# Kernel tuning notes

Measured on AMD Instinct MI355X. Metric: run time of the kernel, lower is better.

## Reference

```python
import jax, jax.numpy as jnp
import numpy as np

BN_EPS = 1e-5


def setup_inputs() -> dict:
    key = jax.random.key(0)
    ks = jax.random.split(key, 6)
    B, N, M, C1, C2 = 8, 8192, 2048, 128, 256
    in_ch = C1 + C2  # 384
    return {
        "xyz1": jax.random.uniform(ks[0], (B, N, 3), dtype=jnp.float32),
        "xyz2": jax.random.uniform(ks[1], (B, M, 3), dtype=jnp.float32),
        "features1": jax.random.normal(ks[2], (B, C1, N), dtype=jnp.float32),
        "features2": jax.random.normal(ks[3], (B, C2, M), dtype=jnp.float32),
        # Conv1d(kernel_size=1, bias=False) weights, squeezed to [out, in]
        "conv_w0": jax.random.normal(ks[4], (256, in_ch), dtype=jnp.float32) * 0.05,
        "gamma0": jnp.ones((256,), dtype=jnp.float32),
        "beta0": jnp.zeros((256,), dtype=jnp.float32),
        "conv_w1": jax.random.normal(ks[5], (256, 256), dtype=jnp.float32) * 0.05,
        "gamma1": jnp.ones((256,), dtype=jnp.float32),
        "beta1": jnp.zeros((256,), dtype=jnp.float32),
    }


def _conv_bn_relu(x, w, gamma, beta):
    # 1x1 Conv1d (no bias) == per-point channel matmul: [B,Cin,N] -> [B,Cout,N]
    x = jnp.einsum("oc,bcn->bon", w, x)
    # BatchNorm1d in training mode: batch stats over (B, N), biased variance
    mu = jnp.mean(x, axis=(0, 2), keepdims=True)
    var = jnp.var(x, axis=(0, 2), keepdims=True)
    x = (x - mu) * jax.lax.rsqrt(var + BN_EPS)
    x = x * gamma[None, :, None] + beta[None, :, None]
    return jax.nn.relu(x)


def reference(xyz1, xyz2, features1, features2,
              conv_w0, gamma0, beta0, conv_w1, gamma1, beta1):
    # squared pairwise distances [B, N, M] (broadcast diff reduced over coord dim)
    diff = xyz1[:, :, None, :] - xyz2[:, None, :, :]  # [B,N,M,3]
    dists = jnp.sum(diff * diff, axis=-1)             # [B,N,M]
    idx = jnp.argmin(dists, axis=-1)                  # [B,N] nearest downsampled point

    # per-batch gather: features2[b, :, idx[b]] -> [B, C2, N]
    interp = jax.vmap(lambda f, i: f[:, i])(features2, idx)

    x = jnp.concatenate([features1, interp], axis=1)  # [B, C1+C2, N]
    x = _conv_bn_relu(x, conv_w0, gamma0, beta0)
    x = _conv_bn_relu(x, conv_w1, gamma1, beta1)
    return x
```

## Files before the change

### kernel.cpp

```cpp
#include <hip/hip_runtime.h>
#include <stdint.h>

typedef unsigned short u16;
typedef unsigned int u32;
typedef __attribute__((ext_vector_type(8))) short short8;
typedef __attribute__((ext_vector_type(4))) float floatx4;

__device__ __forceinline__ u16 f2b(float f) {
  union { float f; u32 u; } c; c.f = f;
  u32 u = c.u;
  u += 0x7fffu + ((u >> 16) & 1u);
  return (u16)(u >> 16);
}
__device__ __forceinline__ float b2f(u16 h) {
  union { u32 u; float f; } c; c.u = ((u32)h) << 16;
  return c.f;
}

__device__ __forceinline__ void glds16(const void* g, void* l) {
  __builtin_amdgcn_global_load_lds((__attribute__((address_space(1))) void*)g,
                                   (__attribute__((address_space(3))) void*)l, 16, 0, 0);
}

__global__ void prep_all_k(const float* __restrict__ xyz1, const float* __restrict__ xyz2,
                           float2* __restrict__ cand,
                           const float* __restrict__ f1, u16* __restrict__ f1t,
                           const float* __restrict__ f2, u16* __restrict__ f2t,
                           const float* __restrict__ w0, u16* __restrict__ w0b,
                           const float* __restrict__ w1, u16* __restrict__ w1b,
                           float* __restrict__ sums) {
  __shared__ __align__(16) char smem[9216];
  int blk = blockIdx.x, t = threadIdx.x;
  if (blk < 512) {
    float4* s2 = (float4*)smem;
    int nq = blk & 7, mq = (blk >> 3) & 7, b = blk >> 6;
    const float* x2 = xyz2 + ((size_t)b * 2048 + mq * 256) * 3;
    s2[t] = make_float4(x2[t * 3], x2[t * 3 + 1], x2[t * 3 + 2], 0.f);
    __syncthreads();
    int n0 = nq * 1024 + t;
    float px[4], py[4], pz[4];
#pragma unroll
    for (int q = 0; q < 4; q++) {
      const float* p1 = xyz1 + ((size_t)b * 8192 + n0 + q * 256) * 3;
      px[q] = p1[0]; py[q] = p1[1]; pz[q] = p1[2];
    }
    float best[4] = {3.0e38f, 3.0e38f, 3.0e38f, 3.0e38f};
    int bi[4] = {0, 0, 0, 0};
#pragma unroll 4
    for (int m = 0; m < 256; m++) {
      float4 qq = s2[m];
#pragma unroll
      for (int q = 0; q < 4; q++) {
        float dx = px[q] - qq.x, dy = py[q] - qq.y, dz = pz[q] - qq.z;
        float d = fmaf(dz, dz, fmaf(dy, dy, dx * dx));
        bool c = d < best[q];
        best[q] = c ? d : best[q];
        bi[q] = c ? m : bi[q];
      }
    }
#pragma unroll
    for (int q = 0; q < 4; q++) {
      int n = n0 + q * 256;
      cand[(size_t)mq * 65536 + (size_t)b * 8192 + n] =
          make_float2(best[q], __int_as_float(mq * 256 + bi[q]));
    }
  } else if (blk < 3584) {
    const float* in; u16* out; int C, N, bx, by, bz;
    if (blk < 2560) { int rel = blk - 512;  in = f1; out = f1t; C = 128; N = 8192; bx = rel & 127; by = (rel >> 7) & 1; bz = rel >> 8; }
    else            { int rel = blk - 2560; in = f2; out = f2t; C = 256; N = 2048; bx = rel & 31;  by = (rel >> 5) & 3; bz = rel >> 7; }
    u16 (*tile)[72] = (u16(*)[72])smem;
    int c0 = by * 64, n0 = bx * 64;
    const float* src = in + ((size_t)bz * C + c0) * N + n0;
#pragma unroll
    for (int i = 0; i < 4; i++) {
      int id = t + i * 256;
      int c = id >> 4, nq = (id & 15) * 4;
      float4 v = *(const float4*)(src + (size_t)c * N + nq);
      tile[nq + 0][c] = f2b(v.x);
      tile[nq + 1][c] = f2b(v.y);
      tile[nq + 2][c] = f2b(v.z);
      tile[nq + 3][c] = f2b(v.w);
    }
    __syncthreads();
    int n = t >> 2, ch = (t & 3) * 16;
    u16* dst = out + ((size_t)bz * N + n0 + n) * C + c0 + ch;
    *(uint4*)dst = *(const uint4*)&tile[n][ch];
    *(uint4*)(dst + 8) = *(const uint4*)&tile[n][ch + 8];
  } else {
    int rel = blk - 3584;
    int i = rel * 256 + t;
    if (rel < 384) w0b[i] = f2b(w0[i]);
    else { int j = i - 98304; w1b[j] = f2b(w1[j]); }
    if (rel < 4) sums[i] = 0.f;
  }
}

__global__ __launch_bounds__(512, 2) void gemm1_k(const u16* __restrict__ w0b, const u16* __restrict__ f1t,
                                                  const u16* __restrict__ f2t, const float2* __restrict__ cand,
                                                  float* __restrict__ sum0, float* __restrict__ sq0,
                                                  u16* __restrict__ y0) {
  __shared__ u16 Aw[128 * 384];
  __shared__ u16 Bs[2][128 * 64];
  int t = threadIdx.x;
  int bid = blockIdx.x;
  int ohalf = (bid >> 3) & 1;
  int pairidx = (bid & 7) | ((bid >> 4) << 3);
  int o0 = ohalf * 128;
  int lane = t & 63, wave = t >> 6;
  int wrow = (wave >> 2) * 64;
  int wp = (wave & 3) * 32;
  int lr = lane & 15, lq = lane >> 4;
  int srow = lane >> 3;
  int sch = ((lane & 7) ^ srow) * 8;

#pragma unroll
  for (int it = 0; it < 12; it++) {
    u32 off = (u32)it * 8192 + (u32)t * 16;
    int row = off / 768;
    int c16 = (off - row * 768) >> 4;
    glds16(w0b + (size_t)(o0 + row) * 384 + ((c16 ^ (row & 7)) << 3),
           (char*)Aw + (size_t)it * 8192 + (size_t)wave * 1024);
  }

  float sa[4][4], qa[4][4];
#pragma unroll
  for (int i = 0; i < 4; i++)
#pragma unroll
    for (int r = 0; r < 4; r++) { sa[i][r] = 0.f; qa[i][r] = 0.f; }

  for (int s = 0; s < 4; s++) {
    int pt = pairidx * 4 + s;
    int pt0 = pt * 128;
    int b = pt0 >> 13;
    int gidx[2];
#pragma unroll
    for (int i = 0; i < 2; i++) {
      int p = pt0 + (wave * 2 + i) * 8 + srow;
      float bd = 3.0e38f; int bi = 0;
#pragma unroll
      for (int qc = 0; qc < 8; qc++) {
        float2 c = cand[(size_t)qc * 65536 + p];
        if (c.x < bd) { bd = c.x; bi = __float_as_int(c.y); }
      }
      gidx[i] = bi;
    }
    floatx4 zero = {0.f, 0.f, 0.f, 0.f};
    floatx4 acc[4][2];
#pragma unroll
    for (int i = 0; i < 4; i++)
#pragma unroll
      for (int j = 0; j < 2; j++) acc[i][j] = zero;

    auto stageB = [&](int k0, int bufi) {
      if (k0 < 128) {
#pragma unroll
        for (int i = 0; i < 2; i++)
          glds16(f1t + (size_t)(pt0 + (wave * 2 + i) * 8 + srow) * 128 + k0 + sch,
                 &Bs[bufi][(wave * 2 + i) * 512]);
      } else {
#pragma unroll
        for (int i = 0; i < 2; i++)
          glds16(f2t + ((size_t)(b << 11) + gidx[i]) * 256 + (k0 - 128) + sch,
                 &Bs[bufi][(wave * 2 + i) * 512]);
      }
    };
    auto compute = [&](int k0, int bufi) {
#pragma unroll
      for (int ks = 0; ks < 2; ks++) {
        short8 af[4], bf[2];
#pragma unroll
        for (int i = 0; i < 4; i++) {
          int row = wrow + i * 16 + lr;
          af[i] = *(const short8*)&Aw[row * 384 + ((((k0 >> 3) + (ks << 2) + lq) ^ (lr & 7)) << 3)];
        }
#pragma unroll
        for (int j = 0; j < 2; j++) {
          int row = wp + j * 16 + lr;
          bf[j] = *(const short8*)&Bs[bufi][row * 64 + ((((ks << 2) | lq) ^ (lr & 7)) << 3)];
        }
#pragma unroll
        for (int i = 0; i < 4; i++)
#pragma unroll
          for (int j = 0; j < 2; j++)
            acc[i][j] = __builtin_amdgcn_mfma_f32_16x16x32_bf16(af[i], bf[j], acc[i][j], 0, 0, 0);
      }
    };

    stageB(0, 0);
    __syncthreads();
#pragma unroll
    for (int k0i = 0; k0i < 6; k0i++) {
      if (k0i < 5) stageB((k0i + 1) * 64, (k0i + 1) & 1);
      compute(k0i * 64, k0i & 1);
      __syncthreads();
    }

#pragma unroll
    for (int i = 0; i < 4; i++) {
#pragma unroll
      for (int j = 0; j < 2; j++) {
        int o = o0 + wrow + i * 16 + lq * 4;
        int p = pt0 + wp + j * 16 + lr;
        uint2 pk;
        pk.x = (u32)f2b(acc[i][j][0]) | ((u32)f2b(acc[i][j][1]) << 16);
        pk.y = (u32)f2b(acc[i][j][2]) | ((u32)f2b(acc[i][j][3]) << 16);
        *(uint2*)&y0[(size_t)p * 256 + o] = pk;
      }
#pragma unroll
      for (int r = 0; r < 4; r++) {
        float v0 = acc[i][0][r], v1 = acc[i][1][r];
        sa[i][r] += v0 + v1;
        qa[i][r] += v0 * v0 + v1 * v1;
      }
    }
  }

#pragma unroll
  for (int i = 0; i < 4; i++)
#pragma unroll
    for (int r = 0; r < 4; r++)
#pragma unroll
      for (int m = 8; m >= 1; m >>= 1) {
        sa[i][r] += __shfl_xor(sa[i][r], m);
        qa[i][r] += __shfl_xor(qa[i][r], m);
      }
  __syncthreads();
  float* red = (float*)&Bs[0][0];
  if (t < 256) red[t] = 0.f;
  __syncthreads();
  if (lr == 0) {
#pragma unroll
    for (int i = 0; i < 4; i++)
#pragma unroll
      for (int r = 0; r < 4; r++) {
        int o = wrow + i * 16 + lq * 4 + r;
        atomicAdd(&red[o], sa[i][r]);
        atomicAdd(&red[128 + o], qa[i][r]);
      }
  }
  __syncthreads();
  if (t < 128) {
    atomicAdd(&sum0[o0 + t], red[t]);
    atomicAdd(&sq0[o0 + t], red[128 + t]);
  }
}

__global__ __launch_bounds__(512, 2) void gemm2_k(const u16* __restrict__ w1b, const u16* __restrict__ y0,
                                                  const float* __restrict__ sum0, const float* __restrict__ sq0,
                                                  const float* __restrict__ gamma0, const float* __restrict__ beta0,
                                                  float* __restrict__ sum1, float* __restrict__ sq1,
                                                  u16* __restrict__ y1) {
  __shared__ u16 Aw[128 * 256];
  __shared__ u16 Bs[2][256 * 64];
  __shared__ float ssc[256], ssh[256];
  int t = threadIdx.x;
  int bid = blockIdx.x;
  int ohalf = (bid >> 3) & 1;
  int pairidx = (bid & 7) | ((bid >> 4) << 3);
  int o0 = ohalf * 128;
  int lane = t & 63, wave = t >> 6;
  int wrow = (wave >> 2) * 64;
  int wp = (wave & 3) * 64;
  int lr = lane & 15, lq = lane >> 4;
  if (t < 256) {
    float mean = sum0[t] * (1.f / 65536.f);
    float var = fmaxf(sq0[t] * (1.f / 65536.f) - mean * mean, 0.f);
    float r = rsqrtf(var + 1e-5f);
    float sc = gamma0[t] * r;
    ssc[t] = sc;
    ssh[t] = beta0[t] - mean * sc;
  }
#pragma unroll
  for (int it = 0; it < 8; it++) {
    u32 off = (u32)it * 8192 + (u32)t * 16;
    int row = off >> 9;
    int c16 = (off & 511) >> 4;
    glds16(w1b + (size_t)(o0 + row) * 256 + ((c16 ^ (row & 7)) << 3),
           (char*)Aw + (size_t)it * 8192 + (size_t)wave * 1024);
  }

  int brow[4], bpc[4], bch[4];
#pragma unroll
  for (int i = 0; i < 4; i++) {
    int id = t + i * 512;
    brow[i] = id >> 3; bpc[i] = id & 7;
    bch[i] = (bpc[i] ^ (brow[i] & 7)) * 8;
  }
  float sa[4][4], qa[4][4];
#pragma unroll
  for (int i = 0; i < 4; i++)
#pragma unroll
    for (int r = 0; r < 4; r++) { sa[i][r] = 0.f; qa[i][r] = 0.f; }

  __syncthreads();

  for (int s = 0; s < 2; s++) {
    int pt0 = (pairidx * 2 + s) * 256;
    uint4 rg[4];
    auto loadB = [&](int k0) {
#pragma unroll
      for (int i = 0; i < 4; i++)
        rg[i] = *(const uint4*)(y0 + (size_t)(pt0 + brow[i]) * 256 + k0 + bch[i]);
    };
    auto xformB = [&](int k0, int bufi) {
#pragma unroll
      for (int i = 0; i < 4; i++) {
        u32 rw[4] = {rg[i].x, rg[i].y, rg[i].z, rg[i].w};
        u32 ow[4];
#pragma unroll
        for (int w = 0; w < 4; w++) {
          int k = k0 + bch[i] + w * 2;
          float v0 = b2f((u16)(rw[w] & 0xffffu));
          float v1 = b2f((u16)(rw[w] >> 16));
          v0 = fmaxf(v0 * ssc[k] + ssh[k], 0.f);
          v1 = fmaxf(v1 * ssc[k + 1] + ssh[k + 1], 0.f);
          ow[w] = (u32)f2b(v0) | ((u32)f2b(v1) << 16);
        }
        uint4 ov; ov.x = ow[0]; ov.y = ow[1]; ov.z = ow[2]; ov.w = ow[3];
        *(uint4*)&Bs[bufi][brow[i] * 64 + bpc[i] * 8] = ov;
      }
    };
    floatx4 zero = {0.f, 0.f, 0.f, 0.f};
    floatx4 acc[4][4];
#pragma unroll
    for (int i = 0; i < 4; i++)
#pragma unroll
      for (int j = 0; j < 4; j++) acc[i][j] = zero;
    auto compute = [&](int k0, int bufi) {
#pragma unroll
      for (int ks = 0; ks < 2; ks++) {
        short8 af[4], bf[4];
#pragma unroll
        for (int i = 0; i < 4; i++) {
          int row = wrow + i * 16 + lr;
          af[i] = *(const short8*)&Aw[row * 256 + ((((k0 >> 3) + (ks << 2) + lq) ^ (lr & 7)) << 3)];
        }
#pragma unroll
        for (int j = 0; j < 4; j++) {
          int row = wp + j * 16 + lr;
          bf[j] = *(const short8*)&Bs[bufi][row * 64 + ((((ks << 2) | lq) ^ (lr & 7)) << 3)];
        }
#pragma unroll
        for (int i = 0; i < 4; i++)
#pragma unroll
          for (int j = 0; j < 4; j++)
            acc[i][j] = __builtin_amdgcn_mfma_f32_16x16x32_bf16(af[i], bf[j], acc[i][j], 0, 0, 0);
      }
    };

    loadB(0);
    xformB(0, 0);
    __syncthreads();
#pragma unroll
    for (int k0i = 0; k0i < 4; k0i++) {
      if (k0i < 3) loadB((k0i + 1) * 64);
      compute(k0i * 64, k0i & 1);
      __syncthreads();
      if (k0i < 3) {
        xformB((k0i + 1) * 64, (k0i + 1) & 1);
        __syncthreads();
      }
    }
#pragma unroll
    for (int i = 0; i < 4; i++) {
#pragma unroll
      for (int j = 0; j < 4; j++) {
        int o = o0 + wrow + i * 16 + lq * 4;
        int p = pt0 + wp + j * 16 + lr;
        uint2 pk;
        pk.x = (u32)f2b(acc[i][j][0]) | ((u32)f2b(acc[i][j][1]) << 16);
        pk.y = (u32)f2b(acc[i][j][2]) | ((u32)f2b(acc[i][j][3]) << 16);
        *(uint2*)&y1[(size_t)p * 256 + o] = pk;
      }
#pragma unroll
      for (int r = 0; r < 4; r++) {
        float v0 = acc[i][0][r], v1 = acc[i][1][r], v2 = acc[i][2][r], v3 = acc[i][3][r];
        sa[i][r] += v0 + v1 + v2 + v3;
        qa[i][r] += v0 * v0 + v1 * v1 + v2 * v2 + v3 * v3;
      }
    }
  }

#pragma unroll
  for (int i = 0; i < 4; i++)
#pragma unroll
    for (int r = 0; r < 4; r++)
#pragma unroll
      for (int m = 8; m >= 1; m >>= 1) {
        sa[i][r] += __shfl_xor(sa[i][r], m);
        qa[i][r] += __shfl_xor(qa[i][r], m);
      }
  __syncthreads();
  float* red = (float*)&Bs[0][0];
  if (t < 256) red[t] = 0.f;
  __syncthreads();
  if (lr == 0) {
#pragma unroll
    for (int i = 0; i < 4; i++)
#pragma unroll
      for (int r = 0; r < 4; r++) {
        int o = wrow + i * 16 + lq * 4 + r;
        atomicAdd(&red[o], sa[i][r]);
        atomicAdd(&red[128 + o], qa[i][r]);
      }
  }
  __syncthreads();
  if (t < 128) {
    atomicAdd(&sum1[o0 + t], red[t]);
    atomicAdd(&sq1[o0 + t], red[128 + t]);
  }
}

__global__ void finalize_k(const u16* __restrict__ y1, const float* __restrict__ sum1,
                           const float* __restrict__ sq1, const float* __restrict__ gamma1,
                           const float* __restrict__ beta1, float* __restrict__ out) {
  __shared__ float tile[64][65];
  __shared__ float fs[64], fh[64];
  int b = blockIdx.z, o0 = blockIdx.y * 64, n0 = blockIdx.x * 64;
  int t = threadIdx.x;
  if (t < 64) {
    int o = o0 + t;
    float mean = sum1[o] * (1.f / 65536.f);
    float var = fmaxf(sq1[o] * (1.f / 65536.f) - mean * mean, 0.f);
    float r = rsqrtf(var + 1e-5f);
    float sc = gamma1[o] * r;
    fs[t] = sc;
    fh[t] = beta1[o] - mean * sc;
  }
  __syncthreads();
  int pl = t >> 2, ch = (t & 3) * 16;
  const u16* src = y1 + ((size_t)(b * 8192 + n0 + pl)) * 256 + o0 + ch;
  uint4 r0 = *(const uint4*)src;
  uint4 r1 = *(const uint4*)(src + 8);
  u16 hv[16];
  *(uint4*)&hv[0] = r0;
  *(uint4*)&hv[8] = r1;
#pragma unroll
  for (int e = 0; e < 16; e++) {
    float v = b2f(hv[e]) * fs[ch + e] + fh[ch + e];
    tile[pl][ch + e] = fmaxf(v, 0.f);
  }
  __syncthreads();
  int ol = t >> 2, nch = (t & 3) * 16;
  float* dst = out + ((size_t)(b * 256 + o0 + ol)) * 8192 + n0 + nch;
#pragma unroll
  for (int j = 0; j < 16; j += 4) {
    float4 v = make_float4(tile[nch + j][ol], tile[nch + j + 1][ol],
                           tile[nch + j + 2][ol], tile[nch + j + 3][ol]);
    *(float4*)(dst + j) = v;
  }
}

extern "C" void kernel_launch(void* const* d_in, const int* in_sizes, int n_in,
                              void* d_out, int out_size, void* d_ws, size_t ws_size,
                              hipStream_t stream) {
  const float* xyz1      = (const float*)d_in[0];
  const float* xyz2      = (const float*)d_in[1];
  const float* features1 = (const float*)d_in[2];
  const float* features2 = (const float*)d_in[3];
  const float* conv_w0   = (const float*)d_in[4];
  const float* gamma0    = (const float*)d_in[5];
  const float* beta0     = (const float*)d_in[6];
  const float* conv_w1   = (const float*)d_in[7];
  const float* gamma1    = (const float*)d_in[8];
  const float* beta1     = (const float*)d_in[9];
  float* out = (float*)d_out;

  char* ws = (char*)d_ws;
  size_t off = 0;
  auto alloc = [&](size_t bytes) {
    char* p = ws + off;
    off = (off + bytes + 4095) & ~(size_t)4095;
    return p;
  };
  float*  sums = (float*)alloc(4 * 256 * 4);
  u16*    w0b  = (u16*)alloc(256 * 384 * 2);
  u16*    w1b  = (u16*)alloc(256 * 256 * 2);
  float2* cand = (float2*)alloc((size_t)8 * 65536 * 8);
  u16*    f1t  = (u16*)alloc((size_t)65536 * 128 * 2);
  u16*    f2t  = (u16*)alloc((size_t)16384 * 256 * 2);
  u16*    y0   = (u16*)alloc((size_t)65536 * 256 * 2);
  u16*    y1   = (u16*)alloc((size_t)65536 * 256 * 2);

  prep_all_k<<<dim3(4224), 256, 0, stream>>>(xyz1, xyz2, cand, features1, f1t,
                                             features2, f2t, conv_w0, w0b, conv_w1, w1b, sums);
  gemm1_k<<<dim3(256), 512, 0, stream>>>(w0b, f1t, f2t, cand, sums + 0, sums + 256, y0);
  gemm2_k<<<dim3(256), 512, 0, stream>>>(w1b, y0, sums + 0, sums + 256, gamma0, beta0,
                                         sums + 512, sums + 768, y1);
  finalize_k<<<dim3(128, 4, 8), 256, 0, stream>>>(y1, sums + 512, sums + 768, gamma1, beta1, out);
}
```

Before: 231.2 us.

## Load B operand fragments directly from global into registers in gemm1

Drops the double-buffered LDS staging of the B tile (point features and gathered interpolated features) in gemm1 and has each lane read its MFMA B fragments straight from global memory. This removes the per-k-step __syncthreads barriers and frees 32KB of LDS, which may allow more occupancy. In exchange, global-load latency is no longer overlapped through async LDS copies, and the waves sharing the same points re-read the same data from global/L2.

After: 270.7 us. +17.1%, slower.

```diff
diff --git a/kernel.cpp b/kernel.cpp
--- a/kernel.cpp
+++ b/kernel.cpp
@@ -100,7 +100,6 @@
                                                   float* __restrict__ sum0, float* __restrict__ sq0,
                                                   u16* __restrict__ y0) {
   __shared__ u16 Aw[128 * 384];
-  __shared__ u16 Bs[2][128 * 64];
   int t = threadIdx.x;
   int bid = blockIdx.x;
   int ohalf = (bid >> 3) & 1;
@@ -110,8 +109,6 @@
   int wrow = (wave >> 2) * 64;
   int wp = (wave & 3) * 32;
   int lr = lane & 15, lq = lane >> 4;
-  int srow = lane >> 3;
-  int sch = ((lane & 7) ^ srow) * 8;
 
 #pragma unroll
   for (int it = 0; it < 12; it++) {
@@ -128,21 +125,22 @@
 #pragma unroll
     for (int r = 0; r < 4; r++) { sa[i][r] = 0.f; qa[i][r] = 0.f; }
 
+  __syncthreads();
+
   for (int s = 0; s < 4; s++) {
-    int pt = pairidx * 4 + s;
-    int pt0 = pt * 128;
+    int pt0 = (pairidx * 4 + s) * 128;
     int b = pt0 >> 13;
     int gidx[2];
 #pragma unroll
-    for (int i = 0; i < 2; i++) {
-      int p = pt0 + (wave * 2 + i) * 8 + srow;
+    for (int j = 0; j < 2; j++) {
+      int p = pt0 + wp + j * 16 + lr;
       float bd = 3.0e38f; int bi = 0;
 #pragma unroll
       for (int qc = 0; qc < 8; qc++) {
         float2 c = cand[(size_t)qc * 65536 + p];
         if (c.x < bd) { bd = c.x; bi = __float_as_int(c.y); }
       }
-      gidx[i] = bi;
+      gidx[j] = bi;
     }
     floatx4 zero = {0.f, 0.f, 0.f, 0.f};
     floatx4 acc[4][2];
@@ -151,48 +149,37 @@
 #pragma unroll
       for (int j = 0; j < 2; j++) acc[i][j] = zero;
 
-    auto stageB = [&](int k0, int bufi) {
-      if (k0 < 128) {
-#pragma unroll
-        for (int i = 0; i < 2; i++)
-          glds16(f1t + (size_t)(pt0 + (wave * 2 + i) * 8 + srow) * 128 + k0 + sch,
-                 &Bs[bufi][(wave * 2 + i) * 512]);
-      } else {
-#pragma unroll
-        for (int i = 0; i < 2; i++)
-          glds16(f2t + ((size_t)(b << 11) + gidx[i]) * 256 + (k0 - 128) + sch,
-                 &Bs[bufi][(wave * 2 + i) * 512]);
-      }
-    };
-    auto compute = [&](int k0, int bufi) {
+#pragma unroll
+    for (int step = 0; step < 6; step++) {
+      short8 bf[2][2];
 #pragma unroll
       for (int ks = 0; ks < 2; ks++) {
-        short8 af[4], bf[2];
+#pragma unroll
+        for (int j = 0; j < 2; j++) {
+          int kk = ks * 32 + lq * 8;
+          if (step < 2) {
+            int p = pt0 + wp + j * 16 + lr;
+            bf[ks][j] = *(const short8*)(f1t + (size_t)p * 128 + step * 64 + kk);
+          } else {
+            bf[ks][j] = *(const short8*)(f2t + ((size_t)(b << 11) + gidx[j]) * 256 +
+                                         (step * 64 - 128) + kk);
+          }
+        }
+      }
+#pragma unroll
+      for (int ks = 0; ks < 2; ks++) {
+        short8 af[4];
 #pragma unroll
         for (int i = 0; i < 4; i++) {
           int row = wrow + i * 16 + lr;
-          af[i] = *(const short8*)&Aw[row * 384 + ((((k0 >> 3) + (ks << 2) + lq) ^ (lr & 7)) << 3)];
+          af[i] = *(const short8*)&Aw[row * 384 + (((step * 8 + (ks << 2) + lq) ^ (lr & 7)) << 3)];
         }
 #pragma unroll
-        for (int j = 0; j < 2; j++) {
-          int row = wp + j * 16 + lr;
-          bf[j] = *(const short8*)&Bs[bufi][row * 64 + ((((ks << 2) | lq) ^ (lr & 7)) << 3)];
-        }
-#pragma unroll
         for (int i = 0; i < 4; i++)
 #pragma unroll
           for (int j = 0; j < 2; j++)
-            acc[i][j] = __builtin_amdgcn_mfma_f32_16x16x32_bf16(af[i], bf[j], acc[i][j], 0, 0, 0);
-      }
-    };
-
-    stageB(0, 0);
-    __syncthreads();
-#pragma unroll
-    for (int k0i = 0; k0i < 6; k0i++) {
-      if (k0i < 5) stageB((k0i + 1) * 64, (k0i + 1) & 1);
-      compute(k0i * 64, k0i & 1);
-      __syncthreads();
+            acc[i][j] = __builtin_amdgcn_mfma_f32_16x16x32_bf16(af[i], bf[ks][j], acc[i][j], 0, 0, 0);
+      }
     }
 
 #pragma unroll
@@ -225,7 +212,7 @@
         qa[i][r] += __shfl_xor(qa[i][r], m);
       }
   __syncthreads();
-  float* red = (float*)&Bs[0][0];
+  float* red = (float*)Aw;
   if (t < 256) red[t] = 0.f;
   __syncthreads();
   if (lr == 0) {
```

## Triple-buffer gemm1 B tiles with cross-subtile prefetch and explicit vmcnt waits

Applied to the files above, without the earlier changes.

Restructures gemm1's B-operand pipeline from double to triple buffering. All nearest-neighbor gather indices are computed up front, so loads for the next point subtile can be prefetched across subtile boundaries. Fine-grained s_waitcnt vmcnt waits plus raw barriers and sched_barriers replace the full __syncthreads drain. It also raises LDS use and drops launch bounds to one block per CU, trading occupancy for deeper in-flight loads.

Measured after the change: 231.4 us. Within noise of the previous version (+0.1%).

```diff
diff --git a/kernel.cpp b/kernel.cpp
--- a/kernel.cpp
+++ b/kernel.cpp
@@ -5,6 +5,12 @@
 typedef unsigned int u32;
 typedef __attribute__((ext_vector_type(8))) short short8;
 typedef __attribute__((ext_vector_type(4))) float floatx4;
+
+#define WVM4 asm volatile("s_waitcnt vmcnt(4)" ::: "memory")
+#define WVM2 asm volatile("s_waitcnt vmcnt(2)" ::: "memory")
+#define WVM0 asm volatile("s_waitcnt vmcnt(0)" ::: "memory")
+#define SCHED0() __builtin_amdgcn_sched_barrier(0)
+#define BAR() __builtin_amdgcn_s_barrier()
 
 __device__ __forceinline__ u16 f2b(float f) {
   union { float f; u32 u; } c; c.f = f;
@@ -95,12 +101,12 @@
   }
 }
 
-__global__ __launch_bounds__(512, 2) void gemm1_k(const u16* __restrict__ w0b, const u16* __restrict__ f1t,
+__global__ __launch_bounds__(512, 1) void gemm1_k(const u16* __restrict__ w0b, const u16* __restrict__ f1t,
                                                   const u16* __restrict__ f2t, const float2* __restrict__ cand,
                                                   float* __restrict__ sum0, float* __restrict__ sq0,
                                                   u16* __restrict__ y0) {
   __shared__ u16 Aw[128 * 384];
-  __shared__ u16 Bs[2][128 * 64];
+  __shared__ u16 Bs[3][128 * 64];
   int t = threadIdx.x;
   int bid = blockIdx.x;
   int ohalf = (bid >> 3) & 1;
@@ -122,17 +128,10 @@
            (char*)Aw + (size_t)it * 8192 + (size_t)wave * 1024);
   }
 
-  float sa[4][4], qa[4][4];
-#pragma unroll
-  for (int i = 0; i < 4; i++)
-#pragma unroll
-    for (int r = 0; r < 4; r++) { sa[i][r] = 0.f; qa[i][r] = 0.f; }
-
+  int gidx[4][2];
+#pragma unroll
   for (int s = 0; s < 4; s++) {
-    int pt = pairidx * 4 + s;
-    int pt0 = pt * 128;
-    int b = pt0 >> 13;
-    int gidx[2];
+    int pt0 = (pairidx * 4 + s) * 128;
 #pragma unroll
     for (int i = 0; i < 2; i++) {
       int p = pt0 + (wave * 2 + i) * 8 + srow;
@@ -142,8 +141,37 @@
         float2 c = cand[(size_t)qc * 65536 + p];
         if (c.x < bd) { bd = c.x; bi = __float_as_int(c.y); }
       }
-      gidx[i] = bi;
-    }
+      gidx[s][i] = bi;
+    }
+  }
+
+  float sa[4][4], qa[4][4];
+#pragma unroll
+  for (int i = 0; i < 4; i++)
+#pragma unroll
+    for (int r = 0; r < 4; r++) { sa[i][r] = 0.f; qa[i][r] = 0.f; }
+
+  __syncthreads();
+
+  auto stageT = [&](int T) {
+    int s2 = T / 6, k = T % 6, buf = T % 3;
+    int pt0s = (pairidx * 4 + s2) * 128;
+    size_t bb = (size_t)((pt0s >> 13) << 11);
+#pragma unroll
+    for (int i = 0; i < 2; i++) {
+      int row = (wave * 2 + i) * 8 + srow;
+      const u16* src;
+      if (k < 2) src = f1t + (size_t)(pt0s + row) * 128 + k * 64 + sch;
+      else       src = f2t + (bb + gidx[s2][i]) * 256 + (k * 64 - 128) + sch;
+      glds16(src, &Bs[buf][(wave * 2 + i) * 512]);
+    }
+  };
+
+  stageT(0); stageT(1); stageT(2);
+
+#pragma unroll
+  for (int s = 0; s < 4; s++) {
+    int pt0 = (pairidx * 4 + s) * 128;
     floatx4 zero = {0.f, 0.f, 0.f, 0.f};
     floatx4 acc[4][2];
 #pragma unroll
@@ -151,32 +179,27 @@
 #pragma unroll
       for (int j = 0; j < 2; j++) acc[i][j] = zero;
 
-    auto stageB = [&](int k0, int bufi) {
-      if (k0 < 128) {
-#pragma unroll
-        for (int i = 0; i < 2; i++)
-          glds16(f1t + (size_t)(pt0 + (wave * 2 + i) * 8 + srow) * 128 + k0 + sch,
-                 &Bs[bufi][(wave * 2 + i) * 512]);
-      } else {
-#pragma unroll
-        for (int i = 0; i < 2; i++)
-          glds16(f2t + ((size_t)(b << 11) + gidx[i]) * 256 + (k0 - 128) + sch,
-                 &Bs[bufi][(wave * 2 + i) * 512]);
-      }
-    };
-    auto compute = [&](int k0, int bufi) {
+#pragma unroll
+    for (int k = 0; k < 6; k++) {
+      int T = s * 6 + k;
+      if (T < 22)      { WVM4; }
+      else if (T == 22){ WVM2; }
+      else             { WVM0; }
+      SCHED0();
+      BAR();
+      SCHED0();
 #pragma unroll
       for (int ks = 0; ks < 2; ks++) {
         short8 af[4], bf[2];
 #pragma unroll
         for (int i = 0; i < 4; i++) {
           int row = wrow + i * 16 + lr;
-          af[i] = *(const short8*)&Aw[row * 384 + ((((k0 >> 3) + (ks << 2) + lq) ^ (lr & 7)) << 3)];
+          af[i] = *(const short8*)&Aw[row * 384 + (((k * 8 + (ks << 2) + lq) ^ (lr & 7)) << 3)];
         }
 #pragma unroll
         for (int j = 0; j < 2; j++) {
           int row = wp + j * 16 + lr;
-          bf[j] = *(const short8*)&Bs[bufi][row * 64 + ((((ks << 2) | lq) ^ (lr & 7)) << 3)];
+          bf[j] = *(const short8*)&Bs[T % 3][row * 64 + ((((ks << 2) | lq) ^ (lr & 7)) << 3)];
         }
 #pragma unroll
         for (int i = 0; i < 4; i++)
@@ -184,15 +207,10 @@
           for (int j = 0; j < 2; j++)
             acc[i][j] = __builtin_amdgcn_mfma_f32_16x16x32_bf16(af[i], bf[j], acc[i][j], 0, 0, 0);
       }
-    };
-
-    stageB(0, 0);
-    __syncthreads();
-#pragma unroll
-    for (int k0i = 0; k0i < 6; k0i++) {
-      if (k0i < 5) stageB((k0i + 1) * 64, (k0i + 1) & 1);
-      compute(k0i * 64, k0i & 1);
-      __syncthreads();
+      SCHED0();
+      BAR();
+      SCHED0();
+      if (T + 3 < 24) stageT(T + 3);
     }
 
 #pragma unroll
```
